# Performance work log

Hardware: AMD Instinct MI355X
Metric: run time of the kernel (lower is better)

The kernel has to match this reference:

```python
import jax, jax.numpy as jnp
import numpy as np

C, H, W_IMG = 3, 128, 128
HW = H * W_IMG
OUT_FEATURES = 2048
BATCH = 256


def _build_fc1():
    size_in = 4 + C
    size_out = 2 * H + 2 * W_IMG + C  # 515
    bs = (size_out - C) // 4
    W = np.zeros((size_out, size_in), np.float32)
    b = np.zeros(size_out, np.float32)
    j = np.arange(bs)
    W[j, 0] = 1.0;               b[j] = -(j + 1)
    W[bs + j, 0] = -1.0; W[bs + j, 1] = -1.0; b[bs + j] = j + 2
    W[2 * bs + j, 2] = 1.0;      b[2 * bs + j] = -(j + 1)
    W[3 * bs + j, 2] = -1.0; W[3 * bs + j, 3] = -1.0; b[3 * bs + j] = j + 2
    for c in range(C):
        W[-1 - c, -1 - c] = 1.0
    return W, b, size_out


def _build_fc2(size_in):
    size_out = (size_in - 1) // 2 + C  # 260
    bs = (size_out - C) // 2
    W = np.zeros((size_out, size_in), np.float32)
    b = np.ones(size_out, np.float32)
    j = np.arange(bs)
    for i in range(2):
        W[i * bs + j, 2 * i * bs + j] = -1.0
        W[i * bs + j, 2 * i * bs + bs + j] = -1.0
    for c in range(C):
        W[-1 - c, -1 - c] = 1.0
        b[-1 - c] = 0.0
    return W, b, size_out


def _build_fc3(size_in):
    size_out = HW + HW * C  # 65536
    ibs = (size_in - C) // 2
    bs = size_out // (1 + C)  # = HW
    W = np.zeros((size_out, size_in), np.float32)
    b = np.zeros(size_out, np.float32)
    j = np.arange(bs)
    r = j // W_IMG
    cc = j % W_IMG
    for i in range(1 + C):
        rows = i * bs + j
        W[rows, r] = 1.0
        W[rows, ibs + cc] = 1.0
        if i >= 1:
            W[rows, size_in - i] = 1.0
    b[:bs] = -1.0
    b[bs:] = -2.0
    return W, b, size_out


def _build_fc4_merged(image_flat, model_w, model_b):
    # Sparse fc4 map M: [C*HW, (1+C)*HW]; row c*HW+i has -image[c*HW+i] at col i
    # and 1 at col (c+1)*HW+i. Merged = model_w @ M, built analytically:
    mw3 = model_w.reshape(OUT_FEATURES, C, HW)
    img3 = image_flat.reshape(1, C, HW)
    first_block = -(mw3 * img3).sum(axis=1)           # [out, HW]
    Wm = np.concatenate([first_block, model_w], axis=1)  # [out, (1+C)*HW]
    bm = model_b + model_w @ image_flat
    return Wm.astype(np.float32), bm.astype(np.float32)


def setup_inputs() -> dict:
    key = jax.random.key(0)
    k1, k2, k3, k4 = jax.random.split(key, 4)
    x = jax.random.normal(k1, (BATCH, 4 + C), dtype=jnp.float32)
    image = np.asarray(jax.random.uniform(k2, (C, H, W_IMG), dtype=jnp.float32))
    model_w = np.asarray(jax.random.normal(k3, (OUT_FEATURES, C * HW), dtype=jnp.float32)) * 0.02
    model_b = np.asarray(jax.random.normal(k4, (OUT_FEATURES,), dtype=jnp.float32)) * 0.02

    W1, b1, s1 = _build_fc1()
    W2, b2, s2 = _build_fc2(s1)
    W3, b3, s3 = _build_fc3(s2)
    W4, b4 = _build_fc4_merged(image.reshape(-1), model_w, model_b)
    return {
        "x": x,
        "W1": jnp.asarray(W1), "b1": jnp.asarray(b1),
        "W2": jnp.asarray(W2), "b2": jnp.asarray(b2),
        "W3": jnp.asarray(W3), "b3": jnp.asarray(b3),
        "W4": jnp.asarray(W4), "b4": jnp.asarray(b4),
    }


def reference(x, W1, b1, W2, b2, W3, b3, W4, b4):
    # x: [B, 7]; each layer is relu(W @ x + b), batched as x @ W.T + b
    h = jax.nn.relu(x @ W1.T + b1)          # [B, 515]
    h = jax.nn.relu(h @ W2.T + b2)          # [B, 260]
    h = jax.nn.relu(h @ W3.T + b3)          # [B, 65536]
    out = jax.nn.relu(h @ W4.T + b4)        # [B, 2048]  (is_cnn=False)
    return out
```

## Files before the change

kernel.cpp:

```cpp
#include <hip/hip_runtime.h>
#include <hip/hip_bf16.h>
#include <stdint.h>

#define BATCH 256
#define NOUT  2048
#define KDIM  65536
#define BN 64
#define BK 32
#define NSPLIT 8
#define NR_CAP 15

typedef __attribute__((ext_vector_type(8))) short bf16x8;
typedef __attribute__((ext_vector_type(4))) float f32x4;
typedef __attribute__((ext_vector_type(2))) unsigned int u32x2;

__device__ __forceinline__ unsigned short f2bf(float f) {
  union { float f; unsigned int u; } v; v.f = f;
  unsigned int r = v.u + 0x7FFFu + ((v.u >> 16) & 1u);
  return (unsigned short)(r >> 16);
}

__device__ __forceinline__ void gload_lds16(const void* g, void* l) {
  __builtin_amdgcn_global_load_lds(
      (const __attribute__((address_space(1))) void*)g,
      (__attribute__((address_space(3))) void*)l, 16, 0, 0);
}

__device__ __forceinline__ float trapf(float xa, float xb, float f) {
  return fmaxf(1.f - fmaxf(xa - (f + 1.f), 0.f)
                   - fmaxf(f + 2.f - xa - xb, 0.f), 0.f);
}

__device__ __forceinline__ void support_wave(const float* __restrict__ x, int t,
                                             unsigned long long& mlo_out,
                                             unsigned long long& mhi_out) {
  const int lane = t & 63;
  unsigned long long mlo = 0ull, mhi = 0ull;
#pragma unroll
  for (int q = 0; q < 4; ++q) {
    const int b = lane * 4 + q;
    const float x0 = x[b * 7], x1 = x[b * 7 + 1];
    if (x1 > 0.f) {
      int lo = (int)floorf(x0 - 2.f) + 1; lo = lo < 0 ? 0 : lo;
      int hi = (int)ceilf(x0 + x1 - 1.f) - 1; hi = hi > 127 ? 127 : hi;
      if (lo <= hi) {
        if (lo < 64) {
          const int h = hi < 63 ? hi : 63;
          const unsigned long long up = (h == 63) ? ~0ull : ((1ull << (h + 1)) - 1ull);
          mlo |= up ^ ((1ull << lo) - 1ull);
        }
        if (hi >= 64) {
          const int l2 = lo > 64 ? lo - 64 : 0;
          const int h2 = hi - 64;
          const unsigned long long up = (h2 == 63) ? ~0ull : ((1ull << (h2 + 1)) - 1ull);
          mhi |= up ^ ((1ull << l2) - 1ull);
        }
      }
    }
  }
#pragma unroll
  for (int s = 32; s >= 1; s >>= 1) {
    mlo |= __shfl_xor(mlo, s);
    mhi |= __shfl_xor(mhi, s);
  }
  mlo_out = mlo; mhi_out = mhi;
}

__device__ __forceinline__ int nR_from_masks(unsigned long long mlo,
                                             unsigned long long mhi) {
  const int nn = __popcll(mlo) + __popcll(mhi);
  return nn > NR_CAP ? NR_CAP : nn;
}

__global__ __launch_bounds__(256)
void k_mega(const float* __restrict__ x, const float* __restrict__ W4,
            unsigned short* __restrict__ Bg, unsigned short* __restrict__ A) {
  __shared__ __align__(16) float buf[4096];
  __shared__ f32x4 red[3][256];
  __shared__ float cvb[128], uvb[128];
  __shared__ unsigned short Rs[NR_CAP + 1];
  const int bid = blockIdx.x, t = threadIdx.x;

  unsigned long long mlo, mhi;
  support_wave(x, t, mlo, mhi);
  const int nR = nR_from_masks(mlo, mhi);
  const int K = nR * 512, Ktot = K + 512;
  if (t < 128) {
    const bool set = (t < 64) ? ((mlo >> t) & 1ull) : ((mhi >> (t - 64)) & 1ull);
    if (set) {
      const int rk = (t < 64)
          ? __popcll(mlo & ((1ull << t) - 1ull))
          : __popcll(mlo) + __popcll(mhi & ((1ull << (t - 64)) - 1ull));
      if (rk < NR_CAP) Rs[rk] = (unsigned short)t;
    }
  }
  __syncthreads();

  const int n = bid;
  const int wid = t >> 6;
  const float* wrow = W4 + (size_t)n * KDIM;
  unsigned short* bgrow = Bg + (size_t)n * Ktot;

  const float* src0 = wrow + 16384;
  f32x4 acc[3];
#pragma unroll
  for (int i = 0; i < 3; ++i) acc[i] = (f32x4){0.f, 0.f, 0.f, 0.f};
#pragma unroll 1
  for (int c = 0; c < 12; ++c) {
#pragma unroll
    for (int rd = 0; rd < 4; ++rd) {
      gload_lds16(src0 + c * 4096 + rd * 1024 + t * 4,
                  (char*)buf + rd * 4096 + wid * 1024);
    }
    __syncthreads();
    const int i = c >> 2;
#pragma unroll
    for (int rd = 0; rd < 4; ++rd) {
      const float4 v = *(const float4*)((const char*)buf + rd * 4096 + t * 16);
      acc[i].x += v.x; acc[i].y += v.y; acc[i].z += v.z; acc[i].w += v.w;
    }
    __syncthreads();
  }
  red[0][t] = acc[0]; red[1][t] = acc[1]; red[2][t] = acc[2];
  __syncthreads();
  if (t < 96) {
    const int i = t >> 5, c = t & 31;
    f32x4 s = red[i][c];
#pragma unroll
    for (int q = 1; q < 8; ++q) {
      const f32x4 v = red[i][c + 32 * q];
      s.x += v.x; s.y += v.y; s.z += v.z; s.w += v.w;
    }
    alignas(8) unsigned short o[4] = {f2bf(s.x), f2bf(s.y), f2bf(s.z), f2bf(s.w)};
    *(u32x2*)(bgrow + K + i * 128 + c * 4) = *(const u32x2*)o;
  } else if (t < 128) {
    *(u32x2*)(bgrow + K + 384 + (t - 96) * 4) = (u32x2){0u, 0u};
  }

  for (int kk = t * 4; kk < K; kk += 1024) {
    const int g = kk >> 7, c = kk & 127;
    const int i = g / nR, ridx = g - i * nR;
    const float4 v = *(const float4*)(wrow + i * 16384 + (int)Rs[ridx] * 128 + c);
    alignas(8) unsigned short o[4] = {f2bf(v.x), f2bf(v.y), f2bf(v.z), f2bf(v.w)};
    *(u32x2*)(bgrow + kk) = *(const u32x2*)o;
  }

  if (bid < 256) {
    const int b = bid;
    const float* xb = x + b * 7;
    const float x0 = xb[0], x1 = xb[1], x2 = xb[2], x3 = xb[3];
    float a4r[4];
    a4r[0] = -1.f;
    a4r[1] = fmaxf(xb[6], 0.f) - 2.f;
    a4r[2] = fmaxf(xb[5], 0.f) - 2.f;
    a4r[3] = fmaxf(xb[4], 0.f) - 2.f;
    if (t < 128) {
      const float f = (float)t;
      cvb[t] = trapf(x2, x3, f);
      uvb[t] = trapf(x0, x1, f);
    }
    __syncthreads();
    unsigned short* Ar = A + (size_t)b * Ktot;
    for (int kk = t; kk < K; kk += 256) {
      const int g = kk >> 7, c = kk & 127;
      const int i = g / nR, ridx = g - i * nR;
      const float u = uvb[Rs[ridx]];
      const float v = cvb[c];
      const float ai = a4r[i];
      Ar[kk] = f2bf(fmaxf(ai + u + v, 0.f) - fmaxf(ai + v, 0.f));
    }
    for (int j = t; j < 512; j += 256) {
      unsigned short val = 0;
      if (j < 384) {
        const int i = (j >> 7) + 1, c = j & 127;
        val = f2bf(fmaxf(a4r[i] + cvb[c], 0.f));
      }
      Ar[K + j] = val;
    }
  }
}

__global__ __launch_bounds__(512, 4)
void k_gemm(const float* __restrict__ x, const unsigned short* __restrict__ A,
            const unsigned short* __restrict__ Bg, float* __restrict__ part) {
  __shared__ unsigned short lA[2][128 * 32];
  __shared__ unsigned short lB[2][64 * 32];
  const int tid = threadIdx.x, bid = blockIdx.x;
  unsigned long long mlo, mhi;
  support_wave(x, tid, mlo, mhi);
  const int nR = nR_from_masks(mlo, mhi);
  const int Ktot = (nR + 1) * 512;
  const int L = Ktot >> 3;
  const int NT = L >> 5;
  const int ks = bid & 7, mt = (bid >> 3) & 1, bn = bid >> 4;
  const int wid = tid >> 6, lane = tid & 63;
  const int wm = wid & 3, wn = wid >> 2;
  const int kbase = ks * L;
  const int nbase = bn * BN;
  const int fr = lane & 15, g = lane >> 4;

  const unsigned short* aSrc = A + (size_t)(mt * 128 + (tid >> 2)) * Ktot + kbase
                               + (((tid & 3) ^ ((tid >> 2) & 3)) << 3);
  const int aDst = wid << 10;
  const unsigned short* bSrc = Bg + (size_t)(nbase + (tid >> 2)) * Ktot + kbase
                               + (((tid & 3) ^ ((tid >> 2) & 3)) << 3);
  const int bDst = (tid >> 6) << 10;

  f32x4 acc[2][2];
#pragma unroll
  for (int mi = 0; mi < 2; ++mi)
#pragma unroll
    for (int ni = 0; ni < 2; ++ni)
      acc[mi][ni] = (f32x4){0.f, 0.f, 0.f, 0.f};
  const int swz = (g ^ (fr & 3)) << 4;

  {
    gload_lds16(aSrc, (char*)lA[0] + aDst);
    if (tid < 256) gload_lds16(bSrc, (char*)lB[0] + bDst);
  }
  __syncthreads();

  for (int kt = 0; kt < NT; ++kt) {
    const int cur = kt & 1, nxt = cur ^ 1;
    const bool more = (kt + 1 < NT);
    if (more) {
      const int kc = (kt + 1) * BK;
      gload_lds16(aSrc + kc, (char*)lA[nxt] + aDst);
      if (tid < 256) gload_lds16(bSrc + kc, (char*)lB[nxt] + bDst);
    }
    const char* bA = (const char*)lA[cur];
    const char* bB = (const char*)lB[cur];
    bf16x8 bfrag[2];
#pragma unroll
    for (int ni = 0; ni < 2; ++ni)
      bfrag[ni] = *(const bf16x8*)(bB + (wn * 32 + ni * 16 + fr) * 64 + swz);
#pragma unroll
    for (int mi = 0; mi < 2; ++mi) {
      const bf16x8 afrag = *(const bf16x8*)(bA + (wm * 32 + mi * 16 + fr) * 64 + swz);
#pragma unroll
      for (int ni = 0; ni < 2; ++ni)
        acc[mi][ni] = __builtin_amdgcn_mfma_f32_16x16x32_bf16(afrag, bfrag[ni],
                                                              acc[mi][ni], 0, 0, 0);
    }
    __syncthreads();
  }

  float* pbase = part + ((size_t)ks << 19);
#pragma unroll
  for (int mi = 0; mi < 2; ++mi) {
#pragma unroll
    for (int ni = 0; ni < 2; ++ni) {
      const int col  = nbase + wn * 32 + ni * 16 + fr;
      const int row0 = mt * 128 + wm * 32 + mi * 16 + (g << 2);
      float* dst = pbase + (size_t)row0 * NOUT + col;
#pragma unroll
      for (int rr = 0; rr < 4; ++rr)
        dst[(size_t)rr * NOUT] = acc[mi][ni][rr];
    }
  }
}

__global__ void k_out(const float* __restrict__ part, const float* __restrict__ b4,
                      float* __restrict__ out) {
  const int i4 = (blockIdx.x * 256 + threadIdx.x) << 2;
  const int n = i4 & (NOUT - 1);
  float4 s = *(const float4*)(b4 + n);
#pragma unroll
  for (int ss = 0; ss < NSPLIT; ++ss) {
    const float4 p = *(const float4*)(part + (size_t)ss * (BATCH * NOUT) + i4);
    s.x += p.x; s.y += p.y; s.z += p.z; s.w += p.w;
  }
  float4 r;
  r.x = fmaxf(s.x, 0.f); r.y = fmaxf(s.y, 0.f);
  r.z = fmaxf(s.z, 0.f); r.w = fmaxf(s.w, 0.f);
  *(float4*)(out + i4) = r;
}

extern "C" void kernel_launch(void* const* d_in, const int* in_sizes, int n_in,
                              void* d_out, int out_size, void* d_ws, size_t ws_size,
                              hipStream_t stream) {
  const float* x  = (const float*)d_in[0];
  const float* W4 = (const float*)d_in[7];
  const float* b4 = (const float*)d_in[8];

  char* ws = (char*)d_ws;
  unsigned short* A    = (unsigned short*)(ws + (1u << 20));
  unsigned short* Bg   = (unsigned short*)(ws + (8u << 20));
  float*          part = (float*)(ws + (44u << 20));

  k_mega<<<NOUT, 256, 0, stream>>>(x, W4, Bg, A);
  k_gemm<<<NSPLIT * 2 * (NOUT / BN), 512, 0, stream>>>(x, A, Bg, part);
  k_out <<<512, 256, 0, stream>>>(part, b4, (float*)d_out);
}
```

Measured before the change: 103.4 us.

## Fuse split-K reduction into GEMM via last-block counter; reuse staged W4 tiles

Result: slower. 260.3 us (+151.7%).

```diff
diff --git a/kernel.cpp b/kernel.cpp
--- a/kernel.cpp
+++ b/kernel.cpp
@@ -74,12 +74,13 @@
 
 __global__ __launch_bounds__(256)
 void k_mega(const float* __restrict__ x, const float* __restrict__ W4,
-            unsigned short* __restrict__ Bg, unsigned short* __restrict__ A) {
+            unsigned short* __restrict__ Bg, unsigned short* __restrict__ A,
+            int* __restrict__ cnt) {
   __shared__ __align__(16) float buf[4096];
-  __shared__ f32x4 red[3][256];
   __shared__ float cvb[128], uvb[128];
   __shared__ unsigned short Rs[NR_CAP + 1];
   const int bid = blockIdx.x, t = threadIdx.x;
+  const int wid = t >> 6;
 
   unsigned long long mlo, mhi;
   support_wave(x, t, mlo, mhi);
@@ -94,10 +95,10 @@
       if (rk < NR_CAP) Rs[rk] = (unsigned short)t;
     }
   }
+  if (bid == 0 && t < 64) cnt[t] = 0;
   __syncthreads();
 
   const int n = bid;
-  const int wid = t >> 6;
   const float* wrow = W4 + (size_t)n * KDIM;
   unsigned short* bgrow = Bg + (size_t)n * Ktot;
 
@@ -108,10 +109,9 @@
 #pragma unroll 1
   for (int c = 0; c < 12; ++c) {
 #pragma unroll
-    for (int rd = 0; rd < 4; ++rd) {
+    for (int rd = 0; rd < 4; ++rd)
       gload_lds16(src0 + c * 4096 + rd * 1024 + t * 4,
                   (char*)buf + rd * 4096 + wid * 1024);
-    }
     __syncthreads();
     const int i = c >> 2;
 #pragma unroll
@@ -119,28 +119,37 @@
       const float4 v = *(const float4*)((const char*)buf + rd * 4096 + t * 16);
       acc[i].x += v.x; acc[i].y += v.y; acc[i].z += v.z; acc[i].w += v.w;
     }
+#pragma unroll 1
+    for (int ridx = 0; ridx < nR; ++ridx) {
+      const int rloc = (int)Rs[ridx] - (c & 3) * 32;
+      if (rloc >= 0 && rloc < 32 && t < 32) {
+        const float4 v = *(const float4*)(buf + (rloc >> 3) * 1024 + (rloc & 7) * 128 + t * 4);
+        alignas(8) unsigned short o[4] = {f2bf(v.x), f2bf(v.y), f2bf(v.z), f2bf(v.w)};
+        *(u32x2*)(bgrow + ((i + 1) * nR + ridx) * 128 + t * 4) = *(const u32x2*)o;
+      }
+    }
     __syncthreads();
   }
-  red[0][t] = acc[0]; red[1][t] = acc[1]; red[2][t] = acc[2];
+  f32x4* red = (f32x4*)buf;
+  red[0 * 256 + t] = acc[0]; red[1 * 256 + t] = acc[1]; red[2 * 256 + t] = acc[2];
   __syncthreads();
   if (t < 96) {
-    const int i = t >> 5, c = t & 31;
-    f32x4 s = red[i][c];
+    const int i = t >> 5, cc = t & 31;
+    f32x4 s = red[i * 256 + cc];
 #pragma unroll
     for (int q = 1; q < 8; ++q) {
-      const f32x4 v = red[i][c + 32 * q];
+      const f32x4 v = red[i * 256 + cc + 32 * q];
       s.x += v.x; s.y += v.y; s.z += v.z; s.w += v.w;
     }
     alignas(8) unsigned short o[4] = {f2bf(s.x), f2bf(s.y), f2bf(s.z), f2bf(s.w)};
-    *(u32x2*)(bgrow + K + i * 128 + c * 4) = *(const u32x2*)o;
+    *(u32x2*)(bgrow + K + i * 128 + cc * 4) = *(const u32x2*)o;
   } else if (t < 128) {
     *(u32x2*)(bgrow + K + 384 + (t - 96) * 4) = (u32x2){0u, 0u};
   }
 
-  for (int kk = t * 4; kk < K; kk += 1024) {
-    const int g = kk >> 7, c = kk & 127;
-    const int i = g / nR, ridx = g - i * nR;
-    const float4 v = *(const float4*)(wrow + i * 16384 + (int)Rs[ridx] * 128 + c);
+  for (int kk = t * 4; kk < nR * 128; kk += 1024) {
+    const int ridx = kk >> 7, cc = kk & 127;
+    const float4 v = *(const float4*)(wrow + (int)Rs[ridx] * 128 + cc);
     alignas(8) unsigned short o[4] = {f2bf(v.x), f2bf(v.y), f2bf(v.z), f2bf(v.w)};
     *(u32x2*)(bgrow + kk) = *(const u32x2*)o;
   }
@@ -162,18 +171,18 @@
     __syncthreads();
     unsigned short* Ar = A + (size_t)b * Ktot;
     for (int kk = t; kk < K; kk += 256) {
-      const int g = kk >> 7, c = kk & 127;
+      const int g = kk >> 7, cc = kk & 127;
       const int i = g / nR, ridx = g - i * nR;
       const float u = uvb[Rs[ridx]];
-      const float v = cvb[c];
+      const float v = cvb[cc];
       const float ai = a4r[i];
       Ar[kk] = f2bf(fmaxf(ai + u + v, 0.f) - fmaxf(ai + v, 0.f));
     }
     for (int j = t; j < 512; j += 256) {
       unsigned short val = 0;
       if (j < 384) {
-        const int i = (j >> 7) + 1, c = j & 127;
-        val = f2bf(fmaxf(a4r[i] + cvb[c], 0.f));
+        const int i = (j >> 7) + 1, cc = j & 127;
+        val = f2bf(fmaxf(a4r[i] + cvb[cc], 0.f));
       }
       Ar[K + j] = val;
     }
@@ -182,9 +191,12 @@
 
 __global__ __launch_bounds__(512, 4)
 void k_gemm(const float* __restrict__ x, const unsigned short* __restrict__ A,
-            const unsigned short* __restrict__ Bg, float* __restrict__ part) {
+            const unsigned short* __restrict__ Bg, float* __restrict__ part,
+            const float* __restrict__ b4, float* __restrict__ out,
+            int* __restrict__ cnt) {
   __shared__ unsigned short lA[2][128 * 32];
   __shared__ unsigned short lB[2][64 * 32];
+  __shared__ int lastFlag;
   const int tid = threadIdx.x, bid = blockIdx.x;
   unsigned long long mlo, mhi;
   support_wave(x, tid, mlo, mhi);
@@ -258,22 +270,29 @@
         dst[(size_t)rr * NOUT] = acc[mi][ni][rr];
     }
   }
-}
-
-__global__ void k_out(const float* __restrict__ part, const float* __restrict__ b4,
-                      float* __restrict__ out) {
-  const int i4 = (blockIdx.x * 256 + threadIdx.x) << 2;
-  const int n = i4 & (NOUT - 1);
-  float4 s = *(const float4*)(b4 + n);
-#pragma unroll
-  for (int ss = 0; ss < NSPLIT; ++ss) {
-    const float4 p = *(const float4*)(part + (size_t)ss * (BATCH * NOUT) + i4);
-    s.x += p.x; s.y += p.y; s.z += p.z; s.w += p.w;
-  }
-  float4 r;
-  r.x = fmaxf(s.x, 0.f); r.y = fmaxf(s.y, 0.f);
-  r.z = fmaxf(s.z, 0.f); r.w = fmaxf(s.w, 0.f);
-  *(float4*)(out + i4) = r;
+
+  __threadfence();
+  if (tid == 0)
+    lastFlag = (atomicAdd(&cnt[(mt << 5) + bn], 1) == NSPLIT - 1) ? 1 : 0;
+  __syncthreads();
+  if (lastFlag) {
+    __threadfence();
+    for (int e = tid; e < 2048; e += 512) {
+      const int row = mt * 128 + (e >> 4);
+      const int col = nbase + (e & 15) * 4;
+      const size_t off = (size_t)row * NOUT + col;
+      float4 s = *(const float4*)(b4 + col);
+#pragma unroll
+      for (int ss = 0; ss < NSPLIT; ++ss) {
+        const float4 p = *(const float4*)(part + (size_t)ss * (BATCH * NOUT) + off);
+        s.x += p.x; s.y += p.y; s.z += p.z; s.w += p.w;
+      }
+      float4 r;
+      r.x = fmaxf(s.x, 0.f); r.y = fmaxf(s.y, 0.f);
+      r.z = fmaxf(s.z, 0.f); r.w = fmaxf(s.w, 0.f);
+      *(float4*)(out + off) = r;
+    }
+  }
 }
 
 extern "C" void kernel_launch(void* const* d_in, const int* in_sizes, int n_in,
@@ -284,11 +303,12 @@
   const float* b4 = (const float*)d_in[8];
 
   char* ws = (char*)d_ws;
+  int*            cnt  = (int*)(ws);
   unsigned short* A    = (unsigned short*)(ws + (1u << 20));
   unsigned short* Bg   = (unsigned short*)(ws + (8u << 20));
   float*          part = (float*)(ws + (44u << 20));
 
-  k_mega<<<NOUT, 256, 0, stream>>>(x, W4, Bg, A);
-  k_gemm<<<NSPLIT * 2 * (NOUT / BN), 512, 0, stream>>>(x, A, Bg, part);
-  k_out <<<512, 256, 0, stream>>>(part, b4, (float*)d_out);
-}
+  k_mega<<<NOUT, 256, 0, stream>>>(x, W4, Bg, A, cnt);
+  k_gemm<<<NSPLIT * 2 * (NOUT / BN), 512, 0, stream>>>(x, A, Bg, part, b4,
+                                                       (float*)d_out, cnt);
+}
```
